# Optimization experiments

Hardware: AMD Instinct MI355X
Metric: run time of the kernel (lower is better)

Reference implementation:

```python
import jax, jax.numpy as jnp
import numpy as np

N = 4096  # number of nodes (matches fill_max of edge indices)


def _dense(edges, n):
    # edges: [2, E] int; dense {0,1} adjacency. Duplicate edges collapse (set semantics).
    return jnp.zeros((n, n), dtype=jnp.float32).at[edges[0], edges[1]].set(1.0)


def setup_inputs() -> dict:
    key = jax.random.key(0)
    ks = jax.random.split(key, 4)
    E = 200000
    mk = lambda k: jax.random.randint(k, (2, E), 0, N, dtype=jnp.int32)
    return {
        "A_pos_t": mk(ks[0]),
        "A_pos_tp1": mk(ks[1]),
        "A_neg_t": mk(ks[2]),
        "A_neg_tp1": mk(ks[3]),
    }


def reference(A_pos_t, A_pos_tp1, A_neg_t, A_neg_tp1):
    p_t = _dense(A_pos_t, N)
    p1 = _dense(A_pos_tp1, N)
    n_t = _dense(A_neg_t, N)
    n1 = _dense(A_neg_tp1, N)

    # edge_index_diff: set symmetric difference == elementwise xor of {0,1} adjacency
    xor_p = p_t + p1 - 2.0 * p_t * p1
    xor_n = n_t + n1 - 2.0 * n_t * n1

    # Balance theory triangle closure on (tp1) graphs.
    # sign(a,b): +1 if pos edge (pos checked first -> priority), -1 elif neg edge.
    sp = p1                      # positive-sign edge indicator
    sn = n1 * (1.0 - p1)         # negative-sign edge indicator (pos has priority)
    off = 1.0 - jnp.eye(N, dtype=jnp.float32)
    spo = sp * off               # exclude b==a / b==c (triples are distinct)
    sno = sn * off

    # number of 2-paths a->b->c with predicted sign +1 / -1
    M_same = spo @ spo + sno @ sno
    M_diff = spo @ sno + sno @ spo

    # the Python loop only infers edges (a,c) with a < c (orientations (i,j,k),(i,k,j),(j,i,k))
    tri = jnp.triu(jnp.ones((N, N), dtype=jnp.float32), k=1)

    ind_p = M_same * tri * (1.0 - p1)  # skip pairs already positively connected
    ind_n = M_diff * tri * (1.0 - n1)  # skip pairs already negatively connected

    # Output: [2, N, N]; entry = xor indicator + indirect-edge multiplicity count
    return jnp.stack([xor_p + ind_p, xor_n + ind_n])
```

## Files before the change

### kernel.cpp

```cpp
#include <hip/hip_runtime.h>


#define NN 4096
#define NW 128
#define MASK_BYTES ((size_t)NN * NW * 4)
#define MASK_WORDS ((size_t)NN * NW)

typedef unsigned int u32;
typedef __attribute__((ext_vector_type(4))) int int4v;
typedef __attribute__((ext_vector_type(4))) float f32x4;

__device__ __forceinline__ void gload_lds16(const char* g, char* l) {
    __builtin_amdgcn_global_load_lds(
        (const __attribute__((address_space(1))) void*)g,
        (__attribute__((address_space(3))) void*)l, 16, 0, 0);
}


__global__ void zero_ws(int4v* __restrict__ p) {
    p[blockIdx.x * 256 + threadIdx.x] = int4v{0, 0, 0, 0};
}

__global__ void scatter_all(const int* __restrict__ e0, const int* __restrict__ e1,
                            const int* __restrict__ e2, const int* __restrict__ e3,
                            int E0, int E1, int E2, int E3,
                            u32* __restrict__ ws) {
    int i = blockIdx.x * blockDim.x + threadIdx.x;
    u32* Pt = ws + 0 * MASK_WORDS;
    u32* P1 = ws + 1 * MASK_WORDS;
    u32* Nt = ws + 2 * MASK_WORDS;
    u32* N1 = ws + 3 * MASK_WORDS;
    if (i < E0) { int r = e0[i], c = e0[i + E0];
        atomicOr(&Pt[r * NW + (c >> 5)], 1u << (c & 31)); }
    if (i < E1) { int r = e1[i], c = e1[i + E1];
        atomicOr(&P1[r * NW + (c >> 5)], 1u << (c & 31)); }
    if (i < E2) { int r = e2[i], c = e2[i + E2];
        atomicOr(&Nt[r * NW + (c >> 5)], 1u << (c & 31)); }
    if (i < E3) { int r = e3[i], c = e3[i + E3];
        atomicOr(&N1[r * NW + (c >> 5)], 1u << (c & 31)); }
}

__device__ __forceinline__ int4v expand_e(u32 sp, u32 sn) {
    int4v E;
    #pragma unroll
    for (int i = 0; i < 4; i++) {
        u32 p = (((sp >> (4 * i)) & 0xFu) * 0x00204081u) & 0x01010101u;
        u32 n = (((sn >> (4 * i)) & 0xFu) * 0x00204081u) & 0x01010101u;
        E[i] = (int)(p | (n << 5));
    }
    return E;
}

__global__ void build_both(const u32* __restrict__ masks,
                           char* __restrict__ E, char* __restrict__ ET) {
    const u32* P  = masks + 1 * MASK_WORDS;
    const u32* Nm = masks + 3 * MASK_WORDS;
    if (blockIdx.x < 2048) {
        int w = blockIdx.x * 256 + threadIdx.x;
        u32 p = P[w];
        u32 n = Nm[w] & ~p;
        int a = w >> 7, col = w & 127;
        if ((a >> 5) == col) {
            u32 db = 1u << (a & 31);
            p &= ~db; n &= ~db;
        }
        char* dst = E + (size_t)a * NN + col * 32;
        *reinterpret_cast<int4v*>(dst)      = expand_e(p & 0xFFFFu, n & 0xFFFFu);
        *reinterpret_cast<int4v*>(dst + 16) = expand_e(p >> 16, n >> 16);
    } else {
        int gw = (blockIdx.x - 2048) * 4 + (threadIdx.x >> 6);
        int lane = threadIdx.x & 63;
        int ab = gw >> 7;
        int wc = gw & 127;
        u32 pw = P[(ab * 64 + lane) * NW + wc];
        u32 nw = Nm[(ab * 64 + lane) * NW + wc];
        u32 myp = 0, myn = 0;
        #pragma unroll
        for (int j = 0; j < 32; j++) {
            unsigned long long bp = __ballot((pw >> j) & 1u);
            unsigned long long bn = __ballot((nw >> j) & 1u);
            if ((lane & 31) == j) {
                myp = (lane < 32) ? (u32)bp : (u32)(bp >> 32);
                myn = (lane < 32) ? (u32)bn : (u32)(bn >> 32);
            }
        }
        u32 p = myp;
        u32 n = myn & ~p;
        int c = wc * 32 + (lane & 31);
        int abase = ab * 64 + (lane >> 5) * 32;
        if (c >= abase && c < abase + 32) {
            u32 db = 1u << (c - abase);
            p &= ~db; n &= ~db;
        }
        char* dst = ET + (size_t)c * NN + abase;
        *reinterpret_cast<int4v*>(dst)      = expand_e(p & 0xFFFFu, n & 0xFFFFu);
        *reinterpret_cast<int4v*>(dst + 16) = expand_e(p >> 16, n >> 16);
    }
}

__global__ __launch_bounds__(256, 2) void gemm_ep(
    const char* __restrict__ E, const char* __restrict__ ET,
    const u32* __restrict__ Pt, const u32* __restrict__ P1,
    const u32* __restrict__ Nt, const u32* __restrict__ N1,
    float* __restrict__ out)
{
    const int tid = threadIdx.x;
    const size_t plane = (size_t)NN * NN;

    int s_ = ((int)blockIdx.x & 7) * 66 + ((int)blockIdx.x >> 3);
    int by = (int)((65.0f - sqrtf(4225.0f - 8.0f * (float)s_)) * 0.5f);
    if (by > 31) by = 31;
    while (by > 0 && 32 * by - (by * (by - 1)) / 2 > s_) --by;
    while (32 * (by + 1) - ((by + 1) * by) / 2 <= s_) ++by;
    int bx = by + s_ - (32 * by - (by * (by - 1)) / 2);
    const int a0 = by << 7, c0 = bx << 7;

    __shared__ char LB[2][2][16384];

    const int wave = tid >> 6, lane = tid & 63;
    const int wr = (wave >> 1) * 64, wcol = (wave & 1) * 64;
    const int lr = lane & 15, lg = lane >> 4;

    const int srow = tid >> 3;
    const int sslot = tid & 7;
    const int soff = ((sslot ^ (srow & 7)) << 4);
    const char* gA0 = E  + (size_t)(a0 + srow)      * NN + soff;
    const char* gA1 = E  + (size_t)(a0 + 32 + srow) * NN + soff;
    const char* gA2 = E  + (size_t)(a0 + 64 + srow) * NN + soff;
    const char* gA3 = E  + (size_t)(a0 + 96 + srow) * NN + soff;
    const char* gB0 = ET + (size_t)(c0 + srow)      * NN + soff;
    const char* gB1 = ET + (size_t)(c0 + 32 + srow) * NN + soff;
    const char* gB2 = ET + (size_t)(c0 + 64 + srow) * NN + soff;
    const char* gB3 = ET + (size_t)(c0 + 96 + srow) * NN + soff;
    const int t16 = tid * 16;

    int4v acc[4][4];
    int4v zero = {0, 0, 0, 0};
    #pragma unroll
    for (int m = 0; m < 4; m++)
        #pragma unroll
        for (int n = 0; n < 4; n++) acc[m][n] = zero;

    #define STAGE(b, p)                                           \
        do {                                                      \
            const int koff = (p) * 128;                           \
            gload_lds16(gA0 + koff, &LB[b][0][t16]);              \
            gload_lds16(gA1 + koff, &LB[b][0][4096 + t16]);       \
            gload_lds16(gA2 + koff, &LB[b][0][8192 + t16]);       \
            gload_lds16(gA3 + koff, &LB[b][0][12288 + t16]);      \
            gload_lds16(gB0 + koff, &LB[b][1][t16]);              \
            gload_lds16(gB1 + koff, &LB[b][1][4096 + t16]);       \
            gload_lds16(gB2 + koff, &LB[b][1][8192 + t16]);       \
            gload_lds16(gB3 + koff, &LB[b][1][12288 + t16]);      \
        } while (0)

    #define COMPUTE(b)                                                          \
        do {                                                                    \
            _Pragma("unroll")                                                   \
            for (int ks = 0; ks < 2; ks++) {                                    \
                int4v bf[4];                                                    \
                _Pragma("unroll")                                               \
                for (int n = 0; n < 4; n++) {                                   \
                    int rowb = wcol + n * 16 + lr;                              \
                    bf[n] = *reinterpret_cast<const int4v*>(&LB[b][1][          \
                        rowb * 128 + (((ks * 4 + lg) ^ (rowb & 7)) << 4)]);     \
                }                                                               \
                __builtin_amdgcn_s_setprio(1);                                  \
                _Pragma("unroll")                                               \
                for (int m = 0; m < 4; m++) {                                   \
                    int rowa = wr + m * 16 + lr;                                \
                    int4v af = *reinterpret_cast<const int4v*>(&LB[b][0][       \
                        rowa * 128 + (((ks * 4 + lg) ^ (rowa & 7)) << 4)]);     \
                    _Pragma("unroll")                                           \
                    for (int n = 0; n < 4; n++)                                 \
                        acc[m][n] = __builtin_amdgcn_mfma_i32_16x16x64_i8(      \
                            af, bf[n], acc[m][n], 0, 0, 0);                     \
                }                                                               \
                __builtin_amdgcn_s_setprio(0);                                  \
            }                                                                   \
        } while (0)

    if (by != bx) {
        #pragma unroll 4
        for (int pass = 0; pass < 16; ++pass) {
            int e = pass * 1024 + tid * 4;
            int r = e >> 7, cc = e & 127;
            int widx = (c0 + r) * NW + ((a0 + cc) >> 5);
            int sh = cc & 31;
            u32 xp = (P1[widx] ^ Pt[widx]) >> sh;
            u32 xn = (N1[widx] ^ Nt[widx]) >> sh;
            f32x4 o0, o1;
            #pragma unroll
            for (int i = 0; i < 4; i++) {
                o0[i] = (float)((xp >> i) & 1u);
                o1[i] = (float)((xn >> i) & 1u);
            }
            size_t ob = (size_t)(c0 + r) * NN + a0 + cc;
            *reinterpret_cast<f32x4*>(out + ob) = o0;
            *reinterpret_cast<f32x4*>(out + plane + ob) = o1;
        }
    }

    STAGE(0, 0);
    asm volatile("s_waitcnt vmcnt(0)" ::: "memory");
    __builtin_amdgcn_s_barrier();

    int cur = 0;
    for (int p = 0; p < 31; ++p) {
        STAGE(cur ^ 1, p + 1);
        COMPUTE(cur);
        asm volatile("s_waitcnt vmcnt(0)" ::: "memory");
        __builtin_amdgcn_s_barrier();
        cur ^= 1;
    }
    COMPUTE(cur);
    #undef STAGE
    #undef COMPUTE

    #pragma unroll
    for (int m = 0; m < 4; m++) {
        #pragma unroll
        for (int n = 0; n < 4; n++) {
            #pragma unroll
            for (int q = 0; q < 4; q++) {
                int a = a0 + wr + m * 16 + lg * 4 + q;
                int c = c0 + wcol + n * 16 + lr;
                int widx = a * NW + (c >> 5);
                int bit = c & 31;
                u32 p1 = (P1[widx] >> bit) & 1u;
                u32 n1 = (N1[widx] >> bit) & 1u;
                u32 pt = (Pt[widx] >> bit) & 1u;
                u32 nt = (Nt[widx] >> bit) & 1u;
                int av = acc[m][n][q];
                int Ms = (av & 31) + (av >> 10);
                int Md = (av >> 5) & 31;
                int o0 = (int)(pt ^ p1) + ((a < c && !p1) ? Ms : 0);
                int o1 = (int)(nt ^ n1) + ((a < c && !n1) ? Md : 0);
                size_t oi = (size_t)a * NN + c;
                out[oi] = (float)o0;
                out[plane + oi] = (float)o1;
            }
        }
    }
}

extern "C" void kernel_launch(void* const* d_in, const int* in_sizes, int n_in,
                              void* d_out, int out_size, void* d_ws, size_t ws_size,
                              hipStream_t stream) {
    char* ws = (char*)d_ws;
    u32* masks = (u32*)ws;
    u32* Pt = masks + 0 * MASK_WORDS;
    u32* P1 = masks + 1 * MASK_WORDS;
    u32* Nt = masks + 2 * MASK_WORDS;
    u32* N1 = masks + 3 * MASK_WORDS;
    char* E  = ws + 4 * MASK_BYTES;
    char* ET = E + (size_t)NN * NN;

    zero_ws<<<2048, 256, 0, stream>>>((int4v*)masks);

    int E0 = in_sizes[0] / 2, E1 = in_sizes[1] / 2;
    int E2 = in_sizes[2] / 2, E3 = in_sizes[3] / 2;
    int Emax = max(max(E0, E1), max(E2, E3));
    scatter_all<<<(Emax + 255) / 256, 256, 0, stream>>>(
        (const int*)d_in[0], (const int*)d_in[1], (const int*)d_in[2],
        (const int*)d_in[3], E0, E1, E2, E3, masks);

    build_both<<<4096, 256, 0, stream>>>(masks, E, ET);

    gemm_ep<<<528, 256, 0, stream>>>(E, ET, Pt, P1, Nt, N1, (float*)d_out);
}
```

Baseline: 131.5 us.

## Replace double-buffered K=128 stages with a 5-slot K=64 ring, prefetch depth 3

The int8 MFMA GEMM main loop now stages 64-wide K tiles into a five-buffer LDS ring instead of two 128-wide buffers. It keeps three tiles in flight and waits with vmcnt(8) instead of draining all loads before each barrier. The goal is to hide global-to-LDS load latency behind MFMA work instead of stalling every iteration. In exchange it uses more LDS (80KB vs 64KB per block) and twice as many barriers. It also switches to a new 4-slot XOR swizzle for the 64-byte rows, which may change LDS bank-conflict behaviour.

Result: slower. 139.9 us (+6.4%).

```diff
diff --git a/kernel.cpp b/kernel.cpp
--- a/kernel.cpp
+++ b/kernel.cpp
@@ -115,24 +115,17 @@
     int bx = by + s_ - (32 * by - (by * (by - 1)) / 2);
     const int a0 = by << 7, c0 = bx << 7;
 
-    __shared__ char LB[2][2][16384];
+    __shared__ char LB[5][16384];
 
     const int wave = tid >> 6, lane = tid & 63;
     const int wr = (wave >> 1) * 64, wcol = (wave & 1) * 64;
     const int lr = lane & 15, lg = lane >> 4;
 
-    const int srow = tid >> 3;
-    const int sslot = tid & 7;
-    const int soff = ((sslot ^ (srow & 7)) << 4);
-    const char* gA0 = E  + (size_t)(a0 + srow)      * NN + soff;
-    const char* gA1 = E  + (size_t)(a0 + 32 + srow) * NN + soff;
-    const char* gA2 = E  + (size_t)(a0 + 64 + srow) * NN + soff;
-    const char* gA3 = E  + (size_t)(a0 + 96 + srow) * NN + soff;
-    const char* gB0 = ET + (size_t)(c0 + srow)      * NN + soff;
-    const char* gB1 = ET + (size_t)(c0 + 32 + srow) * NN + soff;
-    const char* gB2 = ET + (size_t)(c0 + 64 + srow) * NN + soff;
-    const char* gB3 = ET + (size_t)(c0 + 96 + srow) * NN + soff;
-    const int t16 = tid * 16;
+    const int rh = tid >> 2, ch = tid & 3;
+    const int swz = (ch ^ ((rh >> 1) & 3)) << 4;
+    const char* gA = E  + (size_t)(a0 + rh) * NN + swz;
+    const char* gB = ET + (size_t)(c0 + rh) * NN + swz;
+    const int l16 = tid * 16;
 
     int4v acc[4][4];
     int4v zero = {0, 0, 0, 0};
@@ -141,43 +134,36 @@
         #pragma unroll
         for (int n = 0; n < 4; n++) acc[m][n] = zero;
 
-    #define STAGE(b, p)                                           \
-        do {                                                      \
-            const int koff = (p) * 128;                           \
-            gload_lds16(gA0 + koff, &LB[b][0][t16]);              \
-            gload_lds16(gA1 + koff, &LB[b][0][4096 + t16]);       \
-            gload_lds16(gA2 + koff, &LB[b][0][8192 + t16]);       \
-            gload_lds16(gA3 + koff, &LB[b][0][12288 + t16]);      \
-            gload_lds16(gB0 + koff, &LB[b][1][t16]);              \
-            gload_lds16(gB1 + koff, &LB[b][1][4096 + t16]);       \
-            gload_lds16(gB2 + koff, &LB[b][1][8192 + t16]);       \
-            gload_lds16(gB3 + koff, &LB[b][1][12288 + t16]);      \
+    #define STAGE(b, t)                                                \
+        do {                                                           \
+            const int koff = (t) * 64;                                 \
+            gload_lds16(gA + koff,           &LB[b][l16]);             \
+            gload_lds16(gA + 64 * NN + koff, &LB[b][4096 + l16]);      \
+            gload_lds16(gB + koff,           &LB[b][8192 + l16]);      \
+            gload_lds16(gB + 64 * NN + koff, &LB[b][12288 + l16]);     \
         } while (0)
 
-    #define COMPUTE(b)                                                          \
-        do {                                                                    \
-            _Pragma("unroll")                                                   \
-            for (int ks = 0; ks < 2; ks++) {                                    \
-                int4v bf[4];                                                    \
-                _Pragma("unroll")                                               \
-                for (int n = 0; n < 4; n++) {                                   \
-                    int rowb = wcol + n * 16 + lr;                              \
-                    bf[n] = *reinterpret_cast<const int4v*>(&LB[b][1][          \
-                        rowb * 128 + (((ks * 4 + lg) ^ (rowb & 7)) << 4)]);     \
-                }                                                               \
-                __builtin_amdgcn_s_setprio(1);                                  \
-                _Pragma("unroll")                                               \
-                for (int m = 0; m < 4; m++) {                                   \
-                    int rowa = wr + m * 16 + lr;                                \
-                    int4v af = *reinterpret_cast<const int4v*>(&LB[b][0][       \
-                        rowa * 128 + (((ks * 4 + lg) ^ (rowa & 7)) << 4)]);     \
-                    _Pragma("unroll")                                           \
-                    for (int n = 0; n < 4; n++)                                 \
-                        acc[m][n] = __builtin_amdgcn_mfma_i32_16x16x64_i8(      \
-                            af, bf[n], acc[m][n], 0, 0, 0);                     \
-                }                                                               \
-                __builtin_amdgcn_s_setprio(0);                                  \
-            }                                                                   \
+    #define COMPUTE(b)                                                         \
+        do {                                                                   \
+            int4v bf[4];                                                       \
+            _Pragma("unroll")                                                  \
+            for (int n = 0; n < 4; n++) {                                      \
+                int rowb = wcol + n * 16 + lr;                                 \
+                bf[n] = *reinterpret_cast<const int4v*>(&LB[b][                \
+                    8192 + rowb * 64 + ((lg ^ ((rowb >> 1) & 3)) << 4)]);      \
+            }                                                                  \
+            __builtin_amdgcn_s_setprio(1);                                     \
+            _Pragma("unroll")                                                  \
+            for (int m = 0; m < 4; m++) {                                      \
+                int rowa = wr + m * 16 + lr;                                   \
+                int4v af = *reinterpret_cast<const int4v*>(&LB[b][             \
+                    rowa * 64 + ((lg ^ ((rowa >> 1) & 3)) << 4)]);             \
+                _Pragma("unroll")                                              \
+                for (int n = 0; n < 4; n++)                                    \
+                    acc[m][n] = __builtin_amdgcn_mfma_i32_16x16x64_i8(         \
+                        af, bf[n], acc[m][n], 0, 0, 0);                        \
+            }                                                                  \
+            __builtin_amdgcn_s_setprio(0);                                     \
         } while (0)
 
     if (by != bx) {
@@ -202,17 +188,28 @@
     }
 
     STAGE(0, 0);
+    STAGE(1, 1);
+    STAGE(2, 2);
+    asm volatile("s_waitcnt vmcnt(8)" ::: "memory");
+    __builtin_amdgcn_s_barrier();
+
+    int cur = 0;
+    for (int t = 0; t < 61; ++t) {
+        int nb = cur + 3; if (nb >= 5) nb -= 5;
+        STAGE(nb, t + 3);
+        COMPUTE(cur);
+        asm volatile("s_waitcnt vmcnt(8)" ::: "memory");
+        __builtin_amdgcn_s_barrier();
+        cur = (cur == 4) ? 0 : cur + 1;
+    }
+    COMPUTE(cur);
+    asm volatile("s_waitcnt vmcnt(4)" ::: "memory");
+    __builtin_amdgcn_s_barrier();
+    cur = (cur == 4) ? 0 : cur + 1;
+    COMPUTE(cur);
     asm volatile("s_waitcnt vmcnt(0)" ::: "memory");
     __builtin_amdgcn_s_barrier();
-
-    int cur = 0;
-    for (int p = 0; p < 31; ++p) {
-        STAGE(cur ^ 1, p + 1);
-        COMPUTE(cur);
-        asm volatile("s_waitcnt vmcnt(0)" ::: "memory");
-        __builtin_amdgcn_s_barrier();
-        cur ^= 1;
-    }
+    cur = (cur == 4) ? 0 : cur + 1;
     COMPUTE(cur);
     #undef STAGE
     #undef COMPUTE
```
